# Kernel tuning notes

Hardware: AMD Instinct MI355X
Metric: run time of the kernel (lower is better)

## Reference

```python
import jax, jax.numpy as jnp
import numpy as np

HID = 5120      # hidden_size
QLR = 1536      # q_lora_rank
KVLR = 512      # kv_lora_rank
NOPE = 128      # qk_nope_head_dim
ROPE = 64       # qk_rope_head_dim
VDIM = 128      # v_head_dim
H = 32          # num_local_heads
T = 2048        # tokens (single causal prefill, prefix_len=0)
QKD = NOPE + ROPE
SCALE = QKD ** -0.5
EPS = 1e-6
THETA = 10000.0


def rmsnorm(x, w):
    return x * jax.lax.rsqrt(jnp.mean(x * x, axis=-1, keepdims=True) + EPS) * w


def rope_cos_sin(positions):
    inv_freq = 1.0 / (THETA ** (jnp.arange(0, ROPE, 2, dtype=jnp.float32) / ROPE))
    freqs = positions.astype(jnp.float32)[:, None] * inv_freq  # [T, ROPE/2]
    return jnp.cos(freqs), jnp.sin(freqs)


def apply_rope(x, cos, sin):
    # non-neox (interleaved, GPT-J style) rotation on last dim of size ROPE
    x1 = x[..., ::2]
    x2 = x[..., 1::2]
    o1 = x1 * cos - x2 * sin
    o2 = x2 * cos + x1 * sin
    return jnp.stack([o1, o2], axis=-1).reshape(x.shape)


def setup_inputs() -> dict:
    key = jax.random.key(0)
    ks = jax.random.split(key, 10)
    s = 0.02
    return {
        "hidden_states": jax.random.normal(ks[0], (T, HID), jnp.float32),
        "positions": jnp.arange(T, dtype=jnp.int64),
        "w_q_a": jax.random.normal(ks[1], (HID, QLR), jnp.float32) * s,
        "q_a_ln_w": jnp.ones((QLR,), jnp.float32),
        "w_q_b": jax.random.normal(ks[2], (QLR, H * QKD), jnp.float32) * s,
        "w_kv_a": jax.random.normal(ks[3], (HID, KVLR + ROPE), jnp.float32) * s,
        "kv_a_ln_w": jnp.ones((KVLR,), jnp.float32),
        "w_kc": jax.random.normal(ks[4], (H, NOPE, KVLR), jnp.float32) * s,  # absorbed K weight
        "w_vc": jax.random.normal(ks[5], (H, KVLR, VDIM), jnp.float32) * s,  # absorbed V weight
        "w_o": jax.random.normal(ks[6], (H * VDIM, HID), jnp.float32) * s,
    }


def reference(hidden_states, positions, w_q_a, q_a_ln_w, w_q_b, w_kv_a, kv_a_ln_w, w_kc, w_vc, w_o):
    # --- low-rank Q projection ---
    q = rmsnorm(hidden_states @ w_q_a, q_a_ln_w) @ w_q_b          # [T, H*QKD]
    q = q.reshape(T, H, QKD)
    q_nope, q_pe = q[..., :NOPE], q[..., NOPE:]                   # [T,H,NOPE], [T,H,ROPE]

    # --- absorbed q_nope: project into kv_lora space via w_kc ---
    q_nope_out = jnp.einsum("thd,hdk->thk", q_nope, w_kc)         # [T, H, KVLR]

    # --- latent KV ---
    latent = hidden_states @ w_kv_a                               # [T, KVLR+ROPE]
    v_input = rmsnorm(latent[:, :KVLR], kv_a_ln_w)                # [T, KVLR]
    k_pe = latent[:, KVLR:]                                       # [T, ROPE]

    # --- partial RoPE (non-neox) ---
    cos, sin = rope_cos_sin(positions)                            # [T, ROPE/2]
    q_pe = apply_rope(q_pe, cos[:, None, :], sin[:, None, :])
    k_pe = apply_rope(k_pe, cos, sin)

    q_input = jnp.concatenate([q_nope_out, q_pe], axis=-1)        # [T, H, KVLR+ROPE]
    k_input = jnp.concatenate([v_input, k_pe], axis=-1)           # [T, KVLR+ROPE], shared (MQA)

    # --- causal MQA attention over latent KV ---
    scores = jnp.einsum("thd,sd->hts", q_input, k_input) * SCALE  # [H, T, T]
    causal = jnp.tril(jnp.ones((T, T), dtype=bool))
    scores = jnp.where(causal, scores, -1e30)
    probs = jax.nn.softmax(scores, axis=-1)
    ctx = jnp.einsum("hts,sr->thr", probs, v_input)               # [T, H, KVLR]

    # --- absorbed output projection via w_vc, then o_proj ---
    attn_out = jnp.einsum("thr,hrv->thv", ctx, w_vc).reshape(T, H * VDIM)
    return attn_out @ w_o                                         # [T, HID]
```

## Files before the change

kernel.cpp:

```cpp
#include <hip/hip_runtime.h>

#define T_SEQ 2048
#define HID   5120
#define QLR   1536
#define KVLR  512
#define NOPE  128
#define ROPE_D 64
#define VDIM  128
#define NH    32
#define QKD   192

constexpr float SCALE   = 0.07216878364870323f;
constexpr float EPS_F   = 1e-6f;
constexpr float LN10000 = 9.210340371976184f;

typedef __bf16 bf16x8 __attribute__((ext_vector_type(8)));
typedef float  f32x4  __attribute__((ext_vector_type(4)));

__device__ __forceinline__ unsigned short f2bf(float f) {
  union { float f; unsigned u; } v; v.f = f;
  unsigned u = v.u + 0x7fffu + ((v.u >> 16) & 1u);
  return (unsigned short)(u >> 16);
}
__device__ __forceinline__ float bf2f(unsigned short b) {
  union { unsigned u; float f; } v; v.u = ((unsigned)b) << 16;
  return v.f;
}

__device__ __forceinline__ void glds16(const unsigned short* g, unsigned short* l) {
  __builtin_amdgcn_global_load_lds((const __attribute__((address_space(1))) void*)g,
                                   (__attribute__((address_space(3))) void*)l, 16, 0, 0);
}

__global__ void conv_f2b(const float* __restrict__ in, unsigned short* __restrict__ out, long n) {
  long i = ((long)blockIdx.x * blockDim.x + threadIdx.x) * 4;
  if (i >= n) return;
  float4 v = *(const float4*)(in + i);
  uint2 o;
  o.x = (unsigned)f2bf(v.x) | ((unsigned)f2bf(v.y) << 16);
  o.y = (unsigned)f2bf(v.z) | ((unsigned)f2bf(v.w) << 16);
  *(uint2*)(out + i) = o;
}

__global__ void transpose_f2b(const float* __restrict__ in, unsigned short* __restrict__ out,
                              int R, int C, long inB, long outB) {
  __shared__ float tile[32][33];
  const float* inp = in + (long)blockIdx.z * inB;
  unsigned short* outp = out + (long)blockIdx.z * outB;
  int c0 = blockIdx.x * 32, r0 = blockIdx.y * 32;
  int x = threadIdx.x, y = threadIdx.y;
#pragma unroll
  for (int yy = 0; yy < 32; yy += 8)
    tile[y + yy][x] = inp[(long)(r0 + y + yy) * C + c0 + x];
  __syncthreads();
#pragma unroll
  for (int yy = 0; yy < 32; yy += 8)
    outp[(long)(c0 + y + yy) * R + r0 + x] = f2bf(tile[x][y + yy]);
}

__global__ void rmsnorm_rows(const float* __restrict__ in, const float* __restrict__ w,
                             unsigned short* __restrict__ out, int C) {
  int t = blockIdx.x, tid = threadIdx.x;
  __shared__ float sred[4];
  const float* row = in + (long)t * C;
  float ss = 0.f;
  for (int i = tid; i < C; i += 256) { float v = row[i]; ss += v * v; }
#pragma unroll
  for (int o = 32; o; o >>= 1) ss += __shfl_xor(ss, o);
  if ((tid & 63) == 0) sred[tid >> 6] = ss;
  __syncthreads();
  ss = sred[0] + sred[1] + sred[2] + sred[3];
  float rinv = rsqrtf(ss / (float)C + EPS_F);
  for (int i = tid; i < C; i += 256)
    out[(long)t * C + i] = f2bf(row[i] * rinv * w[i]);
}

__global__ void norm_rope_k(const float* __restrict__ latent, const float* __restrict__ w,
                            unsigned short* __restrict__ k_input, unsigned short* __restrict__ v_t) {
  int t = blockIdx.x, tid = threadIdx.x;
  __shared__ float sred[4];
  const float* row = latent + (long)t * 576;
  float ss = 0.f;
  for (int i = tid; i < 512; i += 256) { float v = row[i]; ss += v * v; }
#pragma unroll
  for (int o = 32; o; o >>= 1) ss += __shfl_xor(ss, o);
  if ((tid & 63) == 0) sred[tid >> 6] = ss;
  __syncthreads();
  ss = sred[0] + sred[1] + sred[2] + sred[3];
  float rinv = rsqrtf(ss * (1.f / 512.f) + EPS_F);
  for (int i = tid; i < 512; i += 256) {
    unsigned short b = f2bf(row[i] * rinv * w[i]);
    k_input[(long)t * 576 + i] = b;
    v_t[(long)i * T_SEQ + t] = b;
  }
  if (tid < 32) {
    float fr = (float)t * expf(-((float)(2 * tid) / 64.f) * LN10000);
    float c = cosf(fr), s = sinf(fr);
    float x1 = row[512 + 2 * tid], x2 = row[512 + 2 * tid + 1];
    k_input[(long)t * 576 + 512 + 2 * tid]     = f2bf(x1 * c - x2 * s);
    k_input[(long)t * 576 + 512 + 2 * tid + 1] = f2bf(x2 * c + x1 * s);
  }
}

__global__ void rope_q(const unsigned short* __restrict__ q, unsigned short* __restrict__ q_input) {
  int idx = blockIdx.x * 256 + threadIdx.x;
  int i = idx & 31, h = (idx >> 5) & 31, t = idx >> 10;
  float fr = (float)t * expf(-((float)(2 * i) / 64.f) * LN10000);
  float c = cosf(fr), s = sinf(fr);
  const unsigned short* qp = q + (long)t * (NH * QKD) + h * QKD + NOPE + 2 * i;
  float x1 = bf2f(qp[0]), x2 = bf2f(qp[1]);
  unsigned short* op = q_input + ((long)h * T_SEQ + t) * 576 + 512 + 2 * i;
  op[0] = f2bf(x1 * c - x2 * s);
  op[1] = f2bf(x2 * c + x1 * s);
}

template <bool OUT_BF16>
__global__ __launch_bounds__(256, 2)
void gemm_bt(const unsigned short* __restrict__ A, const unsigned short* __restrict__ Bt,
             void* __restrict__ Cv, int N, int K,
             long lda, long ldb, long ldc, long bA, long bB, long bC) {
  __shared__ __align__(16) unsigned short sA[128 * 64];
  __shared__ __align__(16) unsigned short sB[128 * 64];
  const int b = blockIdx.z;
  const unsigned short* Ap = A + (long)b * bA;
  const unsigned short* Bp = Bt + (long)b * bB;
  const int m0 = blockIdx.x * 128, n0 = blockIdx.y * 128;
  const int tid = threadIdx.x, lane = tid & 63, w = tid >> 6;
  const int wr = w >> 1, wc = w & 1, lo = lane & 15, hi = lane >> 4;
  f32x4 acc[4][4];
#pragma unroll
  for (int i = 0; i < 4; i++)
#pragma unroll
    for (int j = 0; j < 4; j++) acc[i][j] = (f32x4){0.f, 0.f, 0.f, 0.f};
  const int r0 = tid >> 3, cc = tid & 7;
  for (int k0 = 0; k0 < K; k0 += 64) {
    __syncthreads();
#pragma unroll
    for (int i = 0; i < 4; i++) {
      glds16(Ap + (long)(m0 + i * 32 + r0) * lda + k0 + cc * 8, sA + i * 2048 + w * 512);
      glds16(Bp + (long)(n0 + i * 32 + r0) * ldb + k0 + cc * 8, sB + i * 2048 + w * 512);
    }
    __syncthreads();
#pragma unroll
    for (int s = 0; s < 2; s++) {
      bf16x8 af[4], bfr[4];
#pragma unroll
      for (int mt = 0; mt < 4; mt++)
        af[mt] = *(const bf16x8*)(sA + (wr * 64 + mt * 16 + lo) * 64 + s * 32 + hi * 8);
#pragma unroll
      for (int nt = 0; nt < 4; nt++)
        bfr[nt] = *(const bf16x8*)(sB + (wc * 64 + nt * 16 + lo) * 64 + s * 32 + hi * 8);
#pragma unroll
      for (int mt = 0; mt < 4; mt++)
#pragma unroll
        for (int nt = 0; nt < 4; nt++)
          acc[mt][nt] = __builtin_amdgcn_mfma_f32_16x16x32_bf16(af[mt], bfr[nt], acc[mt][nt], 0, 0, 0);
    }
  }
#pragma unroll
  for (int mt = 0; mt < 4; mt++)
#pragma unroll
    for (int nt = 0; nt < 4; nt++) {
      int col = n0 + wc * 64 + nt * 16 + lo;
      if (col < N) {
#pragma unroll
        for (int r = 0; r < 4; r++) {
          long row = m0 + wr * 64 + mt * 16 + hi * 4 + r;
          float v = acc[mt][nt][r];
          if constexpr (OUT_BF16)
            ((unsigned short*)Cv)[(long)b * bC + row * ldc + col] = f2bf(v);
          else
            ((float*)Cv)[(long)b * bC + row * ldc + col] = v;
        }
      }
    }
}

__global__ __launch_bounds__(256, 2)
void flash_attn(const unsigned short* __restrict__ q_input,
                const unsigned short* __restrict__ k_input,
                const unsigned short* __restrict__ v_t,
                unsigned short* __restrict__ ctx_out) {
  __shared__ __align__(16) unsigned short sK[4 * 64 * 64];
  __shared__ __align__(16) unsigned short sV[4 * 64 * 64];
  const int h = blockIdx.x;
  const int i0 = (31 - blockIdx.y) * 64;
  const int tid = threadIdx.x;
  const int lane = tid & 63, w = tid >> 6;
  const int lo = lane & 15, hi = lane >> 4;
  const int qrow = i0 + w * 16 + lo;

  bf16x8 qf[18];
  {
    const unsigned short* qr = q_input + ((long)h * T_SEQ + qrow) * 576;
#pragma unroll
    for (int i = 0; i < 18; i++) qf[i] = *(const bf16x8*)(qr + i * 32 + hi * 8);
  }
#pragma unroll
  for (int i = 0; i < 18; i++) asm volatile("" : "+v"(qf[i]));

  float l_r = 0.f;
  f32x4 of[32];
#pragma unroll
  for (int o = 0; o < 32; o++) of[o] = (f32x4){0.f, 0.f, 0.f, 0.f};

  int kOff[2], vOff[2];
#pragma unroll
  for (int i = 0; i < 2; i++) {
    int u = w * 128 + i * 64 + lane;
    int sl = (u ^ (u >> 3)) & 7;
    kOff[i] = (u >> 3) * 576 + sl * 8;
    vOff[i] = (u >> 3) * T_SEQ + sl * 8;
  }
  const int sw[2] = { ((0 + hi) ^ (lo & 7)) * 8, ((4 + hi) ^ (lo & 7)) * 8 };
  unsigned short* kdst = sK + w * 1024;
  unsigned short* vdst = sV + w * 1024;
  const unsigned short* kld = sK + lo * 64;
  const unsigned short* vld = sV + lo * 64;

#define STAGE_K(c, base)                                                      \
  {                                                                           \
    unsigned short* d_ = kdst + ((c) & 3) * 4096;                             \
    _Pragma("unroll")                                                         \
    for (int i_ = 0; i_ < 2; i_++)                                            \
      glds16(k_input + (base) + kOff[i_] + (c) * 64, d_ + i_ * 512);          \
  }
#define STAGE_V(ch, jk)                                                       \
  {                                                                           \
    unsigned short* d_ = vdst + ((ch) & 3) * 4096;                            \
    _Pragma("unroll")                                                         \
    for (int i_ = 0; i_ < 2; i_++)                                            \
      glds16(v_t + (long)(ch) * 64 * T_SEQ + vOff[i_] + (jk), d_ + i_ * 512); \
  }
#define WB(N)                                                                 \
  __builtin_amdgcn_sched_barrier(0);                                          \
  asm volatile("s_waitcnt vmcnt(" #N ")" ::: "memory");                       \
  __builtin_amdgcn_s_barrier();                                               \
  __builtin_amdgcn_sched_barrier(0);
#define COMPUTE_K(c)                                                          \
  {                                                                           \
    const unsigned short* kb_ = kld + ((c) & 3) * 4096;                       \
    _Pragma("unroll")                                                         \
    for (int ks_ = 0; ks_ < 2; ks_++)                                         \
      _Pragma("unroll")                                                       \
      for (int nt_ = 0; nt_ < 4; nt_++) {                                     \
        bf16x8 a_ = *(const bf16x8*)(kb_ + nt_ * 1024 + sw[ks_]);             \
        sacc[nt_] = __builtin_amdgcn_mfma_f32_16x16x32_bf16(                  \
            a_, qf[2 * (c) + ks_], sacc[nt_], 0, 0, 0);                       \
      }                                                                       \
  }
#define COMPUTE_V(ch)                                                         \
  {                                                                           \
    const unsigned short* vb_ = vld + ((ch) & 3) * 4096;                      \
    _Pragma("unroll")                                                         \
    for (int kk_ = 0; kk_ < 2; kk_++)                                         \
      _Pragma("unroll")                                                       \
      for (int ot_ = 0; ot_ < 4; ot_++) {                                     \
        bf16x8 b_ = *(const bf16x8*)(vb_ + ot_ * 1024 + sw[kk_]);             \
        of[(ch) * 4 + ot_] = __builtin_amdgcn_mfma_f32_16x16x32_bf16(         \
            pa[kk_], b_, of[(ch) * 4 + ot_], 0, 0, 0);                        \
      }                                                                       \
  }

  STAGE_K(0, 0); STAGE_K(1, 0);

  for (int j0 = 0; j0 <= i0; j0 += 64) {
    const long kcur = (long)j0 * 576;
    const long knxt = kcur + 64 * 576;
    const bool more = (j0 < i0);
    f32x4 sacc[4];
#pragma unroll
    for (int nt = 0; nt < 4; nt++) sacc[nt] = (f32x4){0.f, 0.f, 0.f, 0.f};

    STAGE_K(2, kcur); WB(4); COMPUTE_K(0);
    STAGE_K(3, kcur); WB(4); COMPUTE_K(1);
    STAGE_K(4, kcur); WB(4); COMPUTE_K(2);
    STAGE_K(5, kcur); WB(4); COMPUTE_K(3);
    STAGE_K(6, kcur); WB(4); COMPUTE_K(4);
    STAGE_K(7, kcur); WB(4); COMPUTE_K(5);
    STAGE_K(8, kcur); WB(4); COMPUTE_K(6);
    STAGE_V(0, j0);   WB(4); COMPUTE_K(7);
    STAGE_V(1, j0);   WB(4); COMPUTE_K(8);

    const bool diag = (j0 == i0);
    int D2[4][2];
    float psum = 0.f;
#pragma unroll
    for (int nt = 0; nt < 4; nt++) {
      float pv[4];
#pragma unroll
      for (int r = 0; r < 4; r++) {
        float e = __expf(sacc[nt][r] * SCALE);
        if (diag && (j0 + nt * 16 + hi * 4 + r) > qrow) e = 0.f;
        pv[r] = e;
        psum += e;
      }
      D2[nt][0] = (int)f2bf(pv[0]) | ((int)f2bf(pv[1]) << 16);
      D2[nt][1] = (int)f2bf(pv[2]) | ((int)f2bf(pv[3]) << 16);
    }
    psum += __shfl_xor(psum, 16);
    psum += __shfl_xor(psum, 32);
    l_r += psum;
    bf16x8 pa[2];
    {
      const int s0 = lo + 32 * (hi & 1);
#pragma unroll
      for (int kk = 0; kk < 2; kk++) {
        int d[4];
#pragma unroll
        for (int dd = 0; dd < 2; dd++) {
          int t0 = __shfl(D2[2 * kk][dd], s0);
          int t1 = __shfl(D2[2 * kk + 1][dd], s0);
          d[dd] = (hi >> 1) ? t1 : t0;
          int t2 = __shfl(D2[2 * kk][dd], s0 + 16);
          int t3 = __shfl(D2[2 * kk + 1][dd], s0 + 16);
          d[2 + dd] = (hi >> 1) ? t3 : t2;
        }
        int4 di = {d[0], d[1], d[2], d[3]};
        pa[kk] = *(bf16x8*)&di;
      }
    }
    STAGE_V(2, j0); WB(4); COMPUTE_V(0);
    STAGE_V(3, j0); WB(4); COMPUTE_V(1);
    STAGE_V(4, j0); WB(4); COMPUTE_V(2);
    STAGE_V(5, j0); WB(4); COMPUTE_V(3);
    STAGE_V(6, j0); WB(4); COMPUTE_V(4);
    STAGE_V(7, j0); WB(4); COMPUTE_V(5);
    if (more) { STAGE_K(0, knxt); WB(4); } else { WB(2); }
    COMPUTE_V(6);
    if (more) { STAGE_K(1, knxt); WB(4); } else { WB(0); }
    COMPUTE_V(7);
  }
#undef STAGE_K
#undef STAGE_V
#undef WB
#undef COMPUTE_K
#undef COMPUTE_V

  float linv[4];
#pragma unroll
  for (int r = 0; r < 4; r++) linv[r] = 1.f / __shfl(l_r, hi * 4 + r);
#pragma unroll
  for (int o = 0; o < 32; o++) {
    int vd = o * 16 + lo;
#pragma unroll
    for (int r = 0; r < 4; r++) {
      long row = (long)h * T_SEQ + i0 + w * 16 + hi * 4 + r;
      ctx_out[row * 576 + vd] = f2bf(of[o][r] * linv[r]);
    }
  }
}

extern "C" void kernel_launch(void* const* d_in, const int* in_sizes, int n_in,
                              void* d_out, int out_size, void* d_ws, size_t ws_size,
                              hipStream_t stream) {
  (void)in_sizes; (void)n_in; (void)out_size; (void)ws_size;
  const float* hs    = (const float*)d_in[0];
  const float* wqa   = (const float*)d_in[2];
  const float* qlnw  = (const float*)d_in[3];
  const float* wqb   = (const float*)d_in[4];
  const float* wkva  = (const float*)d_in[5];
  const float* kvlnw = (const float*)d_in[6];
  const float* wkc   = (const float*)d_in[7];
  const float* wvc   = (const float*)d_in[8];
  const float* wo    = (const float*)d_in[9];
  float* out = (float*)d_out;

  char* base = (char*)d_ws;
  size_t off = 0;
  auto alloc = [&](size_t bytes) {
    char* r = base + off;
    off += (bytes + 255) & ~(size_t)255;
    return r;
  };
  unsigned short* hs_b  = (unsigned short*)alloc((size_t)T_SEQ * HID * 2);
  unsigned short* wqaT  = (unsigned short*)alloc((size_t)QLR * HID * 2);
  unsigned short* wqbT  = (unsigned short*)alloc((size_t)NH * QKD * QLR * 2);
  unsigned short* wkvaT = (unsigned short*)alloc((size_t)640 * HID * 2);
  unsigned short* wkcT  = (unsigned short*)alloc((size_t)NH * 512 * 128 * 2);
  unsigned short* wvcT  = (unsigned short*)alloc((size_t)NH * 128 * 512 * 2);
  float*          q_a   = (float*)alloc((size_t)T_SEQ * QLR * 4);
  unsigned short* q_a_n = (unsigned short*)alloc((size_t)T_SEQ * QLR * 2);
  unsigned short* qbuf  = (unsigned short*)alloc((size_t)T_SEQ * NH * QKD * 2);
  float*          latent= (float*)alloc((size_t)T_SEQ * 576 * 4);
  unsigned short* k_inp = (unsigned short*)alloc((size_t)T_SEQ * 576 * 2);
  unsigned short* v_t   = (unsigned short*)alloc((size_t)512 * T_SEQ * 2);
  unsigned short* q_inp = (unsigned short*)alloc((size_t)NH * T_SEQ * 576 * 2);
  unsigned short* woT   = (unsigned short*)base;
  unsigned short* attn  = qbuf;

  dim3 tb(32, 8);
  conv_f2b<<<(T_SEQ * HID) / 1024, 256, 0, stream>>>(hs, hs_b, (long)T_SEQ * HID);
  transpose_f2b<<<dim3(QLR / 32, HID / 32, 1), tb, 0, stream>>>(wqa, wqaT, HID, QLR, 0, 0);
  transpose_f2b<<<dim3(576 / 32, HID / 32, 1), tb, 0, stream>>>(wkva, wkvaT, HID, 576, 0, 0);
  gemm_bt<false><<<dim3(T_SEQ / 128, QLR / 128, 1), 256, 0, stream>>>(
      hs_b, wqaT, q_a, QLR, HID, HID, HID, QLR, 0, 0, 0);
  gemm_bt<false><<<dim3(T_SEQ / 128, 5, 1), 256, 0, stream>>>(
      hs_b, wkvaT, latent, 576, HID, HID, HID, 576, 0, 0, 0);
  rmsnorm_rows<<<T_SEQ, 256, 0, stream>>>(q_a, qlnw, q_a_n, QLR);
  norm_rope_k<<<T_SEQ, 256, 0, stream>>>(latent, kvlnw, k_inp, v_t);
  transpose_f2b<<<dim3((NH * QKD) / 32, QLR / 32, 1), tb, 0, stream>>>(wqb, wqbT, QLR, NH * QKD, 0, 0);
  gemm_bt<true><<<dim3(T_SEQ / 128, (NH * QKD) / 128, 1), 256, 0, stream>>>(
      q_a_n, wqbT, qbuf, NH * QKD, QLR, QLR, QLR, NH * QKD, 0, 0, 0);
  transpose_f2b<<<dim3(512 / 32, 128 / 32, NH), tb, 0, stream>>>(wkc, wkcT, 128, 512, 65536, 65536);
  gemm_bt<true><<<dim3(T_SEQ / 128, 512 / 128, NH), 256, 0, stream>>>(
      qbuf, wkcT, q_inp, 512, 128, NH * QKD, 128, 576, QKD, 65536, (long)T_SEQ * 576);
  rope_q<<<(T_SEQ * NH * 32) / 256, 256, 0, stream>>>(qbuf, q_inp);
  flash_attn<<<dim3(NH, 32), 256, 0, stream>>>(q_inp, k_inp, v_t, q_inp);
  transpose_f2b<<<dim3(128 / 32, 512 / 32, NH), tb, 0, stream>>>(wvc, wvcT, 512, 128, 65536, 65536);
  gemm_bt<true><<<dim3(T_SEQ / 128, 1, NH), 256, 0, stream>>>(
      q_inp, wvcT, attn, 128, 512, 576, 512, NH * VDIM, (long)T_SEQ * 576, 65536, 128);
  transpose_f2b<<<dim3(HID / 32, (NH * VDIM) / 32, 1), tb, 0, stream>>>(wo, woT, NH * VDIM, HID, 0, 0);
  gemm_bt<false><<<dim3(T_SEQ / 128, HID / 128, 1), 256, 0, stream>>>(
      attn, woT, out, HID, NH * VDIM, NH * VDIM, NH * VDIM, HID, 0, 0, 0);
}
```

Before: 992.3 us.

## Share one LDS ring between K and V stages and raise attention occupancy

After: 1.727 ms. 1.74x slower.

```diff
diff --git a/kernel.cpp b/kernel.cpp
--- a/kernel.cpp
+++ b/kernel.cpp
@@ -176,13 +176,12 @@
     }
 }
 
-__global__ __launch_bounds__(256, 2)
+__global__ __launch_bounds__(256, 4)
 void flash_attn(const unsigned short* __restrict__ q_input,
                 const unsigned short* __restrict__ k_input,
                 const unsigned short* __restrict__ v_t,
                 unsigned short* __restrict__ ctx_out) {
-  __shared__ __align__(16) unsigned short sK[4 * 64 * 64];
-  __shared__ __align__(16) unsigned short sV[4 * 64 * 64];
+  __shared__ __align__(16) unsigned short sKV[4 * 64 * 64];
   const int h = blockIdx.x;
   const int i0 = (31 - blockIdx.y) * 64;
   const int tid = threadIdx.x;
@@ -213,21 +212,19 @@
     vOff[i] = (u >> 3) * T_SEQ + sl * 8;
   }
   const int sw[2] = { ((0 + hi) ^ (lo & 7)) * 8, ((4 + hi) ^ (lo & 7)) * 8 };
-  unsigned short* kdst = sK + w * 1024;
-  unsigned short* vdst = sV + w * 1024;
-  const unsigned short* kld = sK + lo * 64;
-  const unsigned short* vld = sV + lo * 64;
-
-#define STAGE_K(c, base)                                                      \
+  int kb0 = 0;
+
+#define BUF(ci) ((kb0 + (ci)) & 3)
+#define STAGE_K(c, ci, base)                                                  \
   {                                                                           \
-    unsigned short* d_ = kdst + ((c) & 3) * 4096;                             \
+    unsigned short* d_ = sKV + BUF(ci) * 4096 + w * 1024;                     \
     _Pragma("unroll")                                                         \
     for (int i_ = 0; i_ < 2; i_++)                                            \
       glds16(k_input + (base) + kOff[i_] + (c) * 64, d_ + i_ * 512);          \
   }
 #define STAGE_V(ch, jk)                                                       \
   {                                                                           \
-    unsigned short* d_ = vdst + ((ch) & 3) * 4096;                            \
+    unsigned short* d_ = sKV + BUF(9 + (ch)) * 4096 + w * 1024;               \
     _Pragma("unroll")                                                         \
     for (int i_ = 0; i_ < 2; i_++)                                            \
       glds16(v_t + (long)(ch) * 64 * T_SEQ + vOff[i_] + (jk), d_ + i_ * 512); \
@@ -239,7 +236,7 @@
   __builtin_amdgcn_sched_barrier(0);
 #define COMPUTE_K(c)                                                          \
   {                                                                           \
-    const unsigned short* kb_ = kld + ((c) & 3) * 4096;                       \
+    const unsigned short* kb_ = sKV + BUF(c) * 4096 + lo * 64;                \
     _Pragma("unroll")                                                         \
     for (int ks_ = 0; ks_ < 2; ks_++)                                         \
       _Pragma("unroll")                                                       \
@@ -251,7 +248,7 @@
   }
 #define COMPUTE_V(ch)                                                         \
   {                                                                           \
-    const unsigned short* vb_ = vld + ((ch) & 3) * 4096;                      \
+    const unsigned short* vb_ = sKV + BUF(9 + (ch)) * 4096 + lo * 64;         \
     _Pragma("unroll")                                                         \
     for (int kk_ = 0; kk_ < 2; kk_++)                                         \
       _Pragma("unroll")                                                       \
@@ -262,7 +259,7 @@
       }                                                                       \
   }
 
-  STAGE_K(0, 0); STAGE_K(1, 0);
+  STAGE_K(0, 0, 0); STAGE_K(1, 1, 0);
 
   for (int j0 = 0; j0 <= i0; j0 += 64) {
     const long kcur = (long)j0 * 576;
@@ -272,15 +269,15 @@
 #pragma unroll
     for (int nt = 0; nt < 4; nt++) sacc[nt] = (f32x4){0.f, 0.f, 0.f, 0.f};
 
-    STAGE_K(2, kcur); WB(4); COMPUTE_K(0);
-    STAGE_K(3, kcur); WB(4); COMPUTE_K(1);
-    STAGE_K(4, kcur); WB(4); COMPUTE_K(2);
-    STAGE_K(5, kcur); WB(4); COMPUTE_K(3);
-    STAGE_K(6, kcur); WB(4); COMPUTE_K(4);
-    STAGE_K(7, kcur); WB(4); COMPUTE_K(5);
-    STAGE_K(8, kcur); WB(4); COMPUTE_K(6);
-    STAGE_V(0, j0);   WB(4); COMPUTE_K(7);
-    STAGE_V(1, j0);   WB(4); COMPUTE_K(8);
+    STAGE_K(2, 2, kcur); WB(4); COMPUTE_K(0);
+    STAGE_K(3, 3, kcur); WB(4); COMPUTE_K(1);
+    STAGE_K(4, 4, kcur); WB(4); COMPUTE_K(2);
+    STAGE_K(5, 5, kcur); WB(4); COMPUTE_K(3);
+    STAGE_K(6, 6, kcur); WB(4); COMPUTE_K(4);
+    STAGE_K(7, 7, kcur); WB(4); COMPUTE_K(5);
+    STAGE_K(8, 8, kcur); WB(4); COMPUTE_K(6);
+    STAGE_V(0, j0);      WB(4); COMPUTE_K(7);
+    STAGE_V(1, j0);      WB(4); COMPUTE_K(8);
 
     const bool diag = (j0 == i0);
     int D2[4][2];
@@ -326,11 +323,13 @@
     STAGE_V(5, j0); WB(4); COMPUTE_V(3);
     STAGE_V(6, j0); WB(4); COMPUTE_V(4);
     STAGE_V(7, j0); WB(4); COMPUTE_V(5);
-    if (more) { STAGE_K(0, knxt); WB(4); } else { WB(2); }
+    if (more) { STAGE_K(0, 17, knxt); WB(4); } else { WB(2); }
     COMPUTE_V(6);
-    if (more) { STAGE_K(1, knxt); WB(4); } else { WB(0); }
+    if (more) { STAGE_K(1, 18, knxt); WB(4); } else { WB(0); }
     COMPUTE_V(7);
-  }
+    kb0 = (kb0 + 1) & 3;
+  }
+#undef BUF
 #undef STAGE_K
 #undef STAGE_V
 #undef WB
```
